# Optimization experiments

Measured on AMD Instinct MI355X. Metric: run time of the kernel, lower is better.

The kernel has to match this reference:

```python
import jax, jax.numpy as jnp
import numpy as np

B, D, H, DH = 2048, 1024, 8, 64  # batch, query_dim, heads, dim_head
INNER = H * DH  # 512


def setup_inputs() -> dict:
    key = jax.random.key(0)
    k0, k1, k2, k3 = jax.random.split(key, 4)
    x = jax.random.normal(k0, (B, D), dtype=jnp.float32)
    Wq = jax.random.normal(k1, (D, INNER), dtype=jnp.float32) * 0.02
    Wkv = jax.random.normal(k2, (D, 2 * INNER), dtype=jnp.float32) * 0.02
    Wout = jax.random.normal(k3, (INNER, D), dtype=jnp.float32) * 0.02
    bout = jnp.zeros((D,), dtype=jnp.float32)
    return {"x": x, "Wq": Wq, "Wkv": Wkv, "Wout": Wout, "bout": bout}


def reference(x, Wq, Wkv, Wout, bout):
    # Faithful to the original: 2D x, attention over the flattened (B*H) axis.
    b = x.shape[0]
    scale = DH ** -0.5
    q = (x @ Wq).reshape(b * H, DH)            # (b h) d
    k, v = jnp.split(x @ Wkv, 2, axis=-1)      # each [b, inner]
    k = k.reshape(b * H, DH)
    v = v.reshape(b * H, DH)
    sim = (q @ k.T) * scale                    # [(b h), (b h)] -- 1 GB intermediate
    attn = jax.nn.softmax(sim, axis=-1)        # dropout_rate = 0 -> identity
    out = (attn @ v).reshape(b, INNER)         # b (h d)
    return out @ Wout + bout                   # project_out path
```

## Files before the change

### kernel.cpp

```cpp
#include <hip/hip_runtime.h>
#include <hip/hip_bf16.h>
#include <stdint.h>


typedef __bf16 bf16_t;
typedef __bf16 bf16x4 __attribute__((ext_vector_type(4)));
typedef __bf16 bf16x8 __attribute__((ext_vector_type(8)));
typedef float floatx4 __attribute__((ext_vector_type(4)));

__device__ __forceinline__ floatx4 mfma16(bf16x8 a, bf16x8 b, floatx4 c) {
    return __builtin_amdgcn_mfma_f32_16x16x32_bf16(a, b, c, 0, 0, 0);
}

__device__ __forceinline__ bf16x8 cvt8(float4 a, float4 b) {
    bf16x8 o;
    o[0] = (bf16_t)a.x; o[1] = (bf16_t)a.y; o[2] = (bf16_t)a.z; o[3] = (bf16_t)a.w;
    o[4] = (bf16_t)b.x; o[5] = (bf16_t)b.y; o[6] = (bf16_t)b.z; o[7] = (bf16_t)b.w;
    return o;
}

__global__ __launch_bounds__(256) void cvt_bf16(const float* __restrict__ src,
                                                bf16_t* __restrict__ dst) {
    int i = (blockIdx.x * 256 + threadIdx.x) * 8;
    *(bf16x8*)(dst + i) = cvt8(*(const float4*)(src + i), *(const float4*)(src + i + 4));
}

__global__ __launch_bounds__(256) void transpose_w(const float* __restrict__ in, int N,
                                                   bf16_t* __restrict__ out, int ldo) {
    __shared__ float tile[32][33];
    int n0 = blockIdx.x * 32, k0 = blockIdx.y * 32;
    int tx = threadIdx.x & 31, ty = threadIdx.x >> 5;
#pragma unroll
    for (int i = 0; i < 32; i += 8)
        tile[ty + i][tx] = in[(size_t)(k0 + ty + i) * N + (n0 + tx)];
    __syncthreads();
#pragma unroll
    for (int i = 0; i < 32; i += 8)
        out[(size_t)(n0 + ty + i) * ldo + (k0 + tx)] = (bf16_t)tile[tx][ty + i];
}

template <int OF32, int MI>
__global__ __launch_bounds__(256) void gemm_bt(const bf16_t* __restrict__ A,
                                               const bf16_t* __restrict__ Bt,
                                               const float* __restrict__ bias,
                                               void* __restrict__ Cout,
                                               bf16_t* __restrict__ VtOut, int vt_col0,
                                               int K, int lda, int ldb, int ldc,
                                               float qscale, int qcols) {
    constexpr int MT = MI * 32;
    constexpr int PA = MT / 64;
    __shared__ bf16_t sA[MT * 64];
    __shared__ bf16_t sB[64 * 64];
    int tid = threadIdx.x;
    int wave = tid >> 6, lane = tid & 63;
    int lm = lane & 15, q = lane >> 4;
    int bm = blockIdx.x * MT, bn = blockIdx.y * 64;
    int wm = (wave >> 1) * (MT / 2), wn = (wave & 1) * 32;

    int c0 = (tid & 3) * 2, c1 = c0 + 1;
    int rA[PA], swA[PA];
    size_t srcA0[PA], srcA1[PA];
#pragma unroll
    for (int p = 0; p < PA; ++p) {
        rA[p] = p * 64 + (tid >> 2);
        swA[p] = rA[p] & 7;
        srcA0[p] = (size_t)(bm + rA[p]) * lda + ((c0 ^ swA[p]) << 3);
        srcA1[p] = (size_t)(bm + rA[p]) * lda + ((c1 ^ swA[p]) << 3);
    }
    int rB = tid >> 2, swB = rB & 7;
    size_t srcB0 = (size_t)(bn + rB) * ldb + ((c0 ^ swB) << 3);
    size_t srcB1 = (size_t)(bn + rB) * ldb + ((c1 ^ swB) << 3);

    floatx4 acc[MI][2];
#pragma unroll
    for (int i = 0; i < MI; ++i)
#pragma unroll
        for (int j = 0; j < 2; ++j) acc[i][j] = (floatx4){0.f, 0.f, 0.f, 0.f};

    bf16x8 pa0[PA], pa1[PA], pb0, pb1;

#pragma unroll
    for (int p = 0; p < PA; ++p) {
        pa0[p] = *(const bf16x8*)(A + srcA0[p]);
        pa1[p] = *(const bf16x8*)(A + srcA1[p]);
    }
    pb0 = *(const bf16x8*)(Bt + srcB0);
    pb1 = *(const bf16x8*)(Bt + srcB1);
#pragma unroll
    for (int p = 0; p < PA; ++p) {
        *(bf16x8*)&sA[p * 4096 + tid * 16] = pa0[p];
        *(bf16x8*)&sA[p * 4096 + tid * 16 + 8] = pa1[p];
    }
    *(bf16x8*)&sB[tid * 16] = pb0;
    *(bf16x8*)&sB[tid * 16 + 8] = pb1;
    __syncthreads();

    for (int k0 = 0; k0 < K; k0 += 64) {
        int kn = (k0 + 64 < K) ? k0 + 64 : 0;
#pragma unroll
        for (int p = 0; p < PA; ++p) {
            pa0[p] = *(const bf16x8*)(A + srcA0[p] + kn);
            pa1[p] = *(const bf16x8*)(A + srcA1[p] + kn);
        }
        pb0 = *(const bf16x8*)(Bt + srcB0 + kn);
        pb1 = *(const bf16x8*)(Bt + srcB1 + kn);

#pragma unroll
        for (int s = 0; s < 2; ++s) {
            int cs = s * 4 + q;
            bf16x8 af[MI], bfr[2];
#pragma unroll
            for (int i = 0; i < MI; ++i) {
                int row = wm + i * 16 + lm;
                af[i] = *(bf16x8*)&sA[row * 64 + ((cs ^ (lm & 7)) << 3)];
            }
#pragma unroll
            for (int j = 0; j < 2; ++j) {
                int row = wn + j * 16 + lm;
                bfr[j] = *(bf16x8*)&sB[row * 64 + ((cs ^ (lm & 7)) << 3)];
            }
#pragma unroll
            for (int i = 0; i < MI; ++i)
#pragma unroll
                for (int j = 0; j < 2; ++j)
                    acc[i][j] = mfma16(af[i], bfr[j], acc[i][j]);
        }

        __syncthreads();
#pragma unroll
        for (int p = 0; p < PA; ++p) {
            *(bf16x8*)&sA[p * 4096 + tid * 16] = pa0[p];
            *(bf16x8*)&sA[p * 4096 + tid * 16 + 8] = pa1[p];
        }
        *(bf16x8*)&sB[tid * 16] = pb0;
        *(bf16x8*)&sB[tid * 16 + 8] = pb1;
        __syncthreads();
    }

#pragma unroll
    for (int i = 0; i < MI; ++i)
#pragma unroll
        for (int j = 0; j < 2; ++j)
#pragma unroll
            for (int r = 0; r < 4; ++r) {
                int row = bm + wm + i * 16 + q * 4 + r;
                int col = bn + wn + j * 16 + lm;
                float v = acc[i][j][r];
                if (col < qcols) v *= qscale;
                if (bias) v += bias[col];
                if (col >= vt_col0) {
                    int cc = col - vt_col0;
                    VtOut[(size_t)(cc & 63) * 16384 + row * 8 + (cc >> 6)] = (bf16_t)v;
                } else {
                    size_t off = (size_t)row * ldc + col;
                    if (OF32) ((float*)Cout)[off] = v;
                    else      ((bf16_t*)Cout)[off] = (bf16_t)v;
                }
            }
}

__global__ __launch_bounds__(256, 4) void flash_attn(const bf16_t* __restrict__ QK,
                                                     const bf16_t* __restrict__ Vt,
                                                     bf16_t* __restrict__ O,
                                                     float* __restrict__ accP,
                                                     float* __restrict__ lP,
                                                     int kps, int nsplit) {
    __shared__ bf16_t sK[64 * 64];
    __shared__ bf16_t sVt[64 * 64];
    __shared__ bf16_t sP[128 * 64];
    int tid = threadIdx.x;
    int wave = tid >> 6, lane = tid & 63;
    int lm = lane & 15, q = lane >> 4;
    int sp = blockIdx.y;
    int qrow0 = blockIdx.x * 128 + wave * 32;

    bf16x8 qf[2][2];
#pragma unroll
    for (int sub = 0; sub < 2; ++sub) {
        int qr = qrow0 + sub * 16 + lm;
        const bf16_t* qp = QK + (size_t)(qr >> 3) * 1024 + (qr & 7) * 64;
        qf[sub][0] = *(const bf16x8*)(qp + q * 8);
        qf[sub][1] = *(const bf16x8*)(qp + 32 + q * 8);
    }

    int sr = tid >> 2;
    int ch0 = (tid & 3) * 2, ch1 = ch0 + 1;
    int swz = sr & 7;
    int ksrcA = (sr >> 3) * 1024 + swz * 64 + 512 + ((ch0 ^ swz) << 3);
    int ksrcB = (sr >> 3) * 1024 + swz * 64 + 512 + ((ch1 ^ swz) << 3);
    size_t vsrcA = (size_t)sr * 16384 + ((ch0 ^ swz) << 3);
    size_t vsrcB = (size_t)sr * 16384 + ((ch1 ^ swz) << 3);
    bf16_t* dK = &sK[tid * 16];
    bf16_t* dV = &sVt[tid * 16];

    int c0 = q ^ (lm & 7);
    int rswz = (((lm >> 2) & 3) << 1) ^ ((lm >> 1) & 1);

    floatx4 acc[2][4];
#pragma unroll
    for (int sub = 0; sub < 2; ++sub)
#pragma unroll
        for (int i = 0; i < 4; ++i) acc[sub][i] = (floatx4){0.f, 0.f, 0.f, 0.f};
    float lacc[2][4] = {{0.f, 0.f, 0.f, 0.f}, {0.f, 0.f, 0.f, 0.f}};

    int kt0 = sp * kps, kend = kt0 + kps;

    bf16x8 krA, krB, vrA, vrB;
    {
        const bf16_t* kb = QK + (size_t)kt0 * 128;
        krA = *(const bf16x8*)(kb + ksrcA);
        krB = *(const bf16x8*)(kb + ksrcB);
        vrA = *(const bf16x8*)(Vt + vsrcA + kt0);
        vrB = *(const bf16x8*)(Vt + vsrcB + kt0);
    }
    *(bf16x8*)dK = krA; *(bf16x8*)(dK + 8) = krB;
    *(bf16x8*)dV = vrA; *(bf16x8*)(dV + 8) = vrB;
    __syncthreads();

    for (int kt = kt0; kt < kend; kt += 64) {
        int ktn = (kt + 64 < kend) ? kt + 64 : kt0;
        const bf16_t* kbn = QK + (size_t)ktn * 128;
        krA = *(const bf16x8*)(kbn + ksrcA);
        krB = *(const bf16x8*)(kbn + ksrcB);
        vrA = *(const bf16x8*)(Vt + vsrcA + ktn);
        vrB = *(const bf16x8*)(Vt + vsrcB + ktn);

        floatx4 s[2][4];
#pragma unroll
        for (int nb = 0; nb < 4; ++nb) {
            int row = (nb * 16 + lm) * 64;
            bf16x8 k0 = *(bf16x8*)&sK[row + (c0 << 3)];
            bf16x8 k1 = *(bf16x8*)&sK[row + ((c0 ^ 4) << 3)];
#pragma unroll
            for (int sub = 0; sub < 2; ++sub) {
                floatx4 a = (floatx4){0.f, 0.f, 0.f, 0.f};
                a = mfma16(qf[sub][0], k0, a);
                a = mfma16(qf[sub][1], k1, a);
                s[sub][nb] = a;
            }
        }

#pragma unroll
        for (int sub = 0; sub < 2; ++sub) {
#pragma unroll
            for (int r = 0; r < 4; ++r)
#pragma unroll
                for (int nb = 0; nb < 4; ++nb) {
                    float pv = __builtin_amdgcn_exp2f(s[sub][nb][r]);
                    s[sub][nb][r] = pv;
                    lacc[sub][r] += pv;
                }
#pragma unroll
            for (int r2 = 0; r2 < 4; ++r2) {
                int rowl = wave * 32 + sub * 16 + q * 4 + r2;
#pragma unroll
                for (int nb = 0; nb < 4; ++nb) {
                    int col = nb * 16 + lm;
                    int kbs = (col >> 3) ^ (q << 1) ^ (r2 >> 1);
                    sP[rowl * 64 + (kbs << 3) + (col & 7)] = (bf16_t)s[sub][nb][r2];
                }
            }
        }

#pragma unroll
        for (int jb = 0; jb < 2; ++jb) {
            bf16x8 bv[4];
#pragma unroll
            for (int nd = 0; nd < 4; ++nd)
                bv[nd] = *(bf16x8*)&sVt[(nd * 16 + lm) * 64 + ((c0 ^ (jb << 2)) << 3)];
#pragma unroll
            for (int sub = 0; sub < 2; ++sub) {
                int rowr = wave * 32 + sub * 16 + lm;
                bf16x8 ap = *(bf16x8*)&sP[rowr * 64 + (((jb * 4 + q) ^ rswz) << 3)];
#pragma unroll
                for (int nd = 0; nd < 4; ++nd)
                    acc[sub][nd] = mfma16(ap, bv[nd], acc[sub][nd]);
            }
        }

        __syncthreads();
        *(bf16x8*)dK = krA; *(bf16x8*)(dK + 8) = krB;
        *(bf16x8*)dV = vrA; *(bf16x8*)(dV + 8) = vrB;
        __syncthreads();
    }

#pragma unroll
    for (int sub = 0; sub < 2; ++sub)
#pragma unroll
        for (int r = 0; r < 4; ++r)
#pragma unroll
            for (int off = 1; off < 16; off <<= 1)
                lacc[sub][r] += __shfl_xor(lacc[sub][r], off);

    if (nsplit == 1) {
#pragma unroll
        for (int sub = 0; sub < 2; ++sub)
#pragma unroll
            for (int r = 0; r < 4; ++r) {
                float inv = 1.f / lacc[sub][r];
                int row = qrow0 + sub * 16 + q * 4 + r;
#pragma unroll
                for (int nd = 0; nd < 4; ++nd)
                    O[(size_t)row * 64 + nd * 16 + lm] = (bf16_t)(acc[sub][nd][r] * inv);
            }
    } else {
#pragma unroll
        for (int sub = 0; sub < 2; ++sub)
#pragma unroll
            for (int r = 0; r < 4; ++r) {
                int row = qrow0 + sub * 16 + q * 4 + r;
                size_t base = ((size_t)sp * 16384 + row) * 64;
#pragma unroll
                for (int nd = 0; nd < 4; ++nd)
                    accP[base + nd * 16 + lm] = acc[sub][nd][r];
                if (lm == 0) lP[sp * 16384 + row] = lacc[sub][r];
            }
    }
}

__global__ __launch_bounds__(256) void merge_attn(const float* __restrict__ accP,
                                                  const float* __restrict__ lP,
                                                  bf16_t* __restrict__ O, int nsplit) {
    int idx = blockIdx.x * 256 + threadIdx.x;
    int row = idx >> 4, dh4 = (idx & 15) * 4;
    float4 num = {0.f, 0.f, 0.f, 0.f};
    float den = 0.f;
    for (int s = 0; s < nsplit; ++s) {
        float4 a = *(const float4*)&accP[((size_t)s * 16384 + row) * 64 + dh4];
        num.x += a.x; num.y += a.y; num.z += a.z; num.w += a.w;
        den += lP[s * 16384 + row];
    }
    float inv = 1.f / den;
    bf16x4 o;
    o[0] = (bf16_t)(num.x * inv); o[1] = (bf16_t)(num.y * inv);
    o[2] = (bf16_t)(num.z * inv); o[3] = (bf16_t)(num.w * inv);
    *(bf16x4*)&O[(size_t)row * 64 + dh4] = o;
}

extern "C" void kernel_launch(void* const* d_in, const int* in_sizes, int n_in,
                              void* d_out, int out_size, void* d_ws, size_t ws_size,
                              hipStream_t stream) {
    const float* x    = (const float*)d_in[0];
    const float* Wq   = (const float*)d_in[1];
    const float* Wkv  = (const float*)d_in[2];
    const float* Wout = (const float*)d_in[3];
    const float* bout = (const float*)d_in[4];

    char* ws = (char*)d_ws;
    bf16_t* QK    = (bf16_t*)ws;
    bf16_t* Vt    = (bf16_t*)(ws + 4194304);
    bf16_t* Ob    = (bf16_t*)(ws + 6291456);
    bf16_t* xb    = (bf16_t*)(ws + 8388608);
    bf16_t* WtQKV = (bf16_t*)(ws + 12582912);
    bf16_t* WtOut = (bf16_t*)(ws + 15728640);
    float*  accP  = (float*)(ws + 16777216);

    int nsplit = (ws_size >= (size_t)16777216 + 8 * 4259840) ? 8
               : (ws_size >= (size_t)16777216 + 4 * 4259840) ? 4
               : (ws_size >= (size_t)16777216 + 2 * 4259840) ? 2 : 1;
    float* lP = (float*)(ws + 16777216 + (size_t)nsplit * 4194304);

    cvt_bf16<<<1024, 256, 0, stream>>>(x, xb);
    transpose_w<<<dim3(16, 32), 256, 0, stream>>>(Wq,   512,  WtQKV,        1024);
    transpose_w<<<dim3(32, 32), 256, 0, stream>>>(Wkv,  1024, WtQKV + 512 * 1024, 1024);
    transpose_w<<<dim3(32, 16), 256, 0, stream>>>(Wout, 1024, WtOut,        512);

    gemm_bt<0, 4><<<dim3(16, 24), 256, 0, stream>>>(
        xb, WtQKV, nullptr, QK, Vt, 1024, 1024, 1024, 1024, 1024,
        0.18033688011112042f, 512);

    flash_attn<<<dim3(128, nsplit), 256, 0, stream>>>(QK, Vt, Ob, accP, lP,
                                                      16384 / nsplit, nsplit);
    if (nsplit > 1)
        merge_attn<<<1024, 256, 0, stream>>>(accP, lP, Ob, nsplit);

    gemm_bt<1, 2><<<dim3(32, 16), 256, 0, stream>>>(
        Ob, WtOut, bout, d_out, nullptr, 1 << 30, 512, 512, 512, 1024,
        1.0f, 0);
}
```

Measured before the change: 208.3 us.

## Double attention query tile per block, fuse prep kernels, shrink QKV GEMM tile

The flash attention kernel now handles 256 query rows per block, 64 per wave instead of 32. Each K/V tile loaded into shared memory is therefore reused across twice as many queries, and the exp/store of scores is fused into the QK^T loop. Occupancy is lowered to 2 blocks per CU and the block grid is halved. The four preprocessing launches (x conversion and three weight transposes) are merged into one kernel to save launch overhead. The QKV GEMM moves to a smaller M tile with more blocks, and the larger accumulator footprint in attention risks register pressure or spills.

New measurement: 198.3 us. 1.05x faster.

```diff
diff --git a/kernel.cpp b/kernel.cpp
--- a/kernel.cpp
+++ b/kernel.cpp
@@ -19,17 +19,11 @@
     return o;
 }
 
-__global__ __launch_bounds__(256) void cvt_bf16(const float* __restrict__ src,
-                                                bf16_t* __restrict__ dst) {
-    int i = (blockIdx.x * 256 + threadIdx.x) * 8;
-    *(bf16x8*)(dst + i) = cvt8(*(const float4*)(src + i), *(const float4*)(src + i + 4));
-}
-
-__global__ __launch_bounds__(256) void transpose_w(const float* __restrict__ in, int N,
-                                                   bf16_t* __restrict__ out, int ldo) {
-    __shared__ float tile[32][33];
-    int n0 = blockIdx.x * 32, k0 = blockIdx.y * 32;
-    int tx = threadIdx.x & 31, ty = threadIdx.x >> 5;
+__device__ __forceinline__ void transpose_body(const float* __restrict__ in, int N,
+                                               bf16_t* __restrict__ out, int ldo,
+                                               int bx, int by, int tid, float (*tile)[33]) {
+    int n0 = bx * 32, k0 = by * 32;
+    int tx = tid & 31, ty = tid >> 5;
 #pragma unroll
     for (int i = 0; i < 32; i += 8)
         tile[ty + i][tx] = in[(size_t)(k0 + ty + i) * N + (n0 + tx)];
@@ -37,6 +31,30 @@
 #pragma unroll
     for (int i = 0; i < 32; i += 8)
         out[(size_t)(n0 + ty + i) * ldo + (k0 + tx)] = (bf16_t)tile[tx][ty + i];
+}
+
+__global__ __launch_bounds__(256) void prep_all(const float* __restrict__ x,
+                                                bf16_t* __restrict__ xb,
+                                                const float* __restrict__ Wq,
+                                                const float* __restrict__ Wkv,
+                                                const float* __restrict__ Wout,
+                                                bf16_t* __restrict__ WtQKV,
+                                                bf16_t* __restrict__ WtOut) {
+    __shared__ float tile[32][33];
+    int b = blockIdx.x, tid = threadIdx.x;
+    if (b < 1024) {
+        int i = (b * 256 + tid) * 8;
+        *(bf16x8*)(xb + i) = cvt8(*(const float4*)(x + i), *(const float4*)(x + i + 4));
+    } else if (b < 1536) {
+        b -= 1024;
+        transpose_body(Wq, 512, WtQKV, 1024, b & 15, b >> 4, tid, tile);
+    } else if (b < 2560) {
+        b -= 1536;
+        transpose_body(Wkv, 1024, WtQKV + 512 * 1024, 1024, b & 31, b >> 5, tid, tile);
+    } else {
+        b -= 2560;
+        transpose_body(Wout, 1024, WtOut, 512, b & 31, b >> 5, tid, tile);
+    }
 }
 
 template <int OF32, int MI>
@@ -78,7 +96,6 @@
         for (int j = 0; j < 2; ++j) acc[i][j] = (floatx4){0.f, 0.f, 0.f, 0.f};
 
     bf16x8 pa0[PA], pa1[PA], pb0, pb1;
-
 #pragma unroll
     for (int p = 0; p < PA; ++p) {
         pa0[p] = *(const bf16x8*)(A + srcA0[p]);
@@ -159,7 +176,7 @@
             }
 }
 
-__global__ __launch_bounds__(256, 4) void flash_attn(const bf16_t* __restrict__ QK,
+__global__ __launch_bounds__(256, 2) void flash_attn(const bf16_t* __restrict__ QK,
                                                      const bf16_t* __restrict__ Vt,
                                                      bf16_t* __restrict__ O,
                                                      float* __restrict__ accP,
@@ -167,16 +184,16 @@
                                                      int kps, int nsplit) {
     __shared__ bf16_t sK[64 * 64];
     __shared__ bf16_t sVt[64 * 64];
-    __shared__ bf16_t sP[128 * 64];
+    __shared__ bf16_t sP[256 * 64];
     int tid = threadIdx.x;
     int wave = tid >> 6, lane = tid & 63;
     int lm = lane & 15, q = lane >> 4;
     int sp = blockIdx.y;
-    int qrow0 = blockIdx.x * 128 + wave * 32;
-
-    bf16x8 qf[2][2];
-#pragma unroll
-    for (int sub = 0; sub < 2; ++sub) {
+    int qrow0 = blockIdx.x * 256 + wave * 64;
+
+    bf16x8 qf[4][2];
+#pragma unroll
+    for (int sub = 0; sub < 4; ++sub) {
         int qr = qrow0 + sub * 16 + lm;
         const bf16_t* qp = QK + (size_t)(qr >> 3) * 1024 + (qr & 7) * 64;
         qf[sub][0] = *(const bf16x8*)(qp + q * 8);
@@ -196,12 +213,16 @@
     int c0 = q ^ (lm & 7);
     int rswz = (((lm >> 2) & 3) << 1) ^ ((lm >> 1) & 1);
 
-    floatx4 acc[2][4];
-#pragma unroll
-    for (int sub = 0; sub < 2; ++sub)
+    floatx4 acc[4][4];
+#pragma unroll
+    for (int sub = 0; sub < 4; ++sub)
 #pragma unroll
         for (int i = 0; i < 4; ++i) acc[sub][i] = (floatx4){0.f, 0.f, 0.f, 0.f};
-    float lacc[2][4] = {{0.f, 0.f, 0.f, 0.f}, {0.f, 0.f, 0.f, 0.f}};
+    float lacc[4][4];
+#pragma unroll
+    for (int sub = 0; sub < 4; ++sub)
+#pragma unroll
+        for (int r = 0; r < 4; ++r) lacc[sub][r] = 0.f;
 
     int kt0 = sp * kps, kend = kt0 + kps;
 
@@ -225,39 +246,28 @@
         vrA = *(const bf16x8*)(Vt + vsrcA + ktn);
         vrB = *(const bf16x8*)(Vt + vsrcB + ktn);
 
-        floatx4 s[2][4];
 #pragma unroll
         for (int nb = 0; nb < 4; ++nb) {
             int row = (nb * 16 + lm) * 64;
             bf16x8 k0 = *(bf16x8*)&sK[row + (c0 << 3)];
             bf16x8 k1 = *(bf16x8*)&sK[row + ((c0 ^ 4) << 3)];
 #pragma unroll
-            for (int sub = 0; sub < 2; ++sub) {
+            for (int sub = 0; sub < 4; ++sub) {
                 floatx4 a = (floatx4){0.f, 0.f, 0.f, 0.f};
                 a = mfma16(qf[sub][0], k0, a);
                 a = mfma16(qf[sub][1], k1, a);
-                s[sub][nb] = a;
-            }
-        }
-
-#pragma unroll
-        for (int sub = 0; sub < 2; ++sub) {
-#pragma unroll
-            for (int r = 0; r < 4; ++r)
-#pragma unroll
-                for (int nb = 0; nb < 4; ++nb) {
-                    float pv = __builtin_amdgcn_exp2f(s[sub][nb][r]);
-                    s[sub][nb][r] = pv;
+#pragma unroll
+                for (int r = 0; r < 4; ++r) {
+                    float pv = __builtin_amdgcn_exp2f(a[r]);
+                    a[r] = pv;
                     lacc[sub][r] += pv;
                 }
 #pragma unroll
-            for (int r2 = 0; r2 < 4; ++r2) {
-                int rowl = wave * 32 + sub * 16 + q * 4 + r2;
-#pragma unroll
-                for (int nb = 0; nb < 4; ++nb) {
+                for (int r2 = 0; r2 < 4; ++r2) {
+                    int rowl = wave * 64 + sub * 16 + q * 4 + r2;
                     int col = nb * 16 + lm;
                     int kbs = (col >> 3) ^ (q << 1) ^ (r2 >> 1);
-                    sP[rowl * 64 + (kbs << 3) + (col & 7)] = (bf16_t)s[sub][nb][r2];
+                    sP[rowl * 64 + (kbs << 3) + (col & 7)] = (bf16_t)a[r2];
                 }
             }
         }
@@ -269,8 +279,8 @@
             for (int nd = 0; nd < 4; ++nd)
                 bv[nd] = *(bf16x8*)&sVt[(nd * 16 + lm) * 64 + ((c0 ^ (jb << 2)) << 3)];
 #pragma unroll
-            for (int sub = 0; sub < 2; ++sub) {
-                int rowr = wave * 32 + sub * 16 + lm;
+            for (int sub = 0; sub < 4; ++sub) {
+                int rowr = wave * 64 + sub * 16 + lm;
                 bf16x8 ap = *(bf16x8*)&sP[rowr * 64 + (((jb * 4 + q) ^ rswz) << 3)];
 #pragma unroll
                 for (int nd = 0; nd < 4; ++nd)
@@ -285,7 +295,7 @@
     }
 
 #pragma unroll
-    for (int sub = 0; sub < 2; ++sub)
+    for (int sub = 0; sub < 4; ++sub)
 #pragma unroll
         for (int r = 0; r < 4; ++r)
 #pragma unroll
@@ -294,7 +304,7 @@
 
     if (nsplit == 1) {
 #pragma unroll
-        for (int sub = 0; sub < 2; ++sub)
+        for (int sub = 0; sub < 4; ++sub)
 #pragma unroll
             for (int r = 0; r < 4; ++r) {
                 float inv = 1.f / lacc[sub][r];
@@ -305,7 +315,7 @@
             }
     } else {
 #pragma unroll
-        for (int sub = 0; sub < 2; ++sub)
+        for (int sub = 0; sub < 4; ++sub)
 #pragma unroll
             for (int r = 0; r < 4; ++r) {
                 int row = qrow0 + sub * 16 + q * 4 + r;
@@ -360,17 +370,14 @@
                : (ws_size >= (size_t)16777216 + 2 * 4259840) ? 2 : 1;
     float* lP = (float*)(ws + 16777216 + (size_t)nsplit * 4194304);
 
-    cvt_bf16<<<1024, 256, 0, stream>>>(x, xb);
-    transpose_w<<<dim3(16, 32), 256, 0, stream>>>(Wq,   512,  WtQKV,        1024);
-    transpose_w<<<dim3(32, 32), 256, 0, stream>>>(Wkv,  1024, WtQKV + 512 * 1024, 1024);
-    transpose_w<<<dim3(32, 16), 256, 0, stream>>>(Wout, 1024, WtOut,        512);
-
-    gemm_bt<0, 4><<<dim3(16, 24), 256, 0, stream>>>(
+    prep_all<<<3072, 256, 0, stream>>>(x, xb, Wq, Wkv, Wout, WtQKV, WtOut);
+
+    gemm_bt<0, 2><<<dim3(32, 24), 256, 0, stream>>>(
         xb, WtQKV, nullptr, QK, Vt, 1024, 1024, 1024, 1024, 1024,
         0.18033688011112042f, 512);
 
-    flash_attn<<<dim3(128, nsplit), 256, 0, stream>>>(QK, Vt, Ob, accP, lP,
-                                                      16384 / nsplit, nsplit);
+    flash_attn<<<dim3(64, nsplit), 256, 0, stream>>>(QK, Vt, Ob, accP, lP,
+                                                     16384 / nsplit, nsplit);
     if (nsplit > 1)
         merge_attn<<<1024, 256, 0, stream>>>(accP, lP, Ob, nsplit);
 
```
